# Kernel optimization log

Hardware: AMD Instinct MI355X
Metric: run time of the kernel (lower is better)

## Reference

```python
import jax, jax.numpy as jnp
import numpy as np

DN = ('NCHW', 'OIHW', 'NCHW')
BLOB_HW = 16  # hard-coded in make_gaussian_blob_maps

_ENC = [(32, 3), (32, 32), (64, 32), (64, 64), (128, 64), (128, 128), (128, 128)]
_DEC = [(64, 128), (64, 64), (32, 64), (32, 32), (16, 32), (16, 16)]


def _conv(x, w, b, stride):
    y = jax.lax.conv_general_dilated(x, w, (stride, stride), 'SAME', dimension_numbers=DN)
    return y + b[None, :, None, None]


def _tconv(x, w, b):
    # decoder stride-2 stage: 'iteratively doubling the input width'
    y = jax.lax.conv_transpose(x, w, (2, 2), 'SAME', dimension_numbers=DN)
    return y + b[None, :, None, None]


def setup_inputs() -> dict:
    key = jax.random.key(0)
    keys = jax.random.split(key, 1 + 2 * (len(_ENC) + len(_DEC)))
    inp = {'x': jax.random.normal(keys[0], (4, 8, 3, 128, 128), jnp.float32)}
    i = 1
    for j, (o, c) in enumerate(_ENC):
        inp[f'enc_w{j}'] = 0.05 * jax.random.normal(keys[i], (o, c, 3, 3), jnp.float32); i += 1
        inp[f'enc_b{j}'] = 0.05 * jax.random.normal(keys[i], (o,), jnp.float32); i += 1
    for j, (o, c) in enumerate(_DEC):
        inp[f'dec_w{j}'] = 0.05 * jax.random.normal(keys[i], (o, c, 3, 3), jnp.float32); i += 1
        inp[f'dec_b{j}'] = 0.05 * jax.random.normal(keys[i], (o,), jnp.float32); i += 1
    return inp


def _forward(x, enc_w0, enc_b0, enc_w1, enc_b1, enc_w2, enc_b2, enc_w3, enc_b3,
             enc_w4, enc_b4, enc_w5, enc_b5, enc_w6, enc_b6,
             dec_w0, dec_b0, dec_w1, dec_b1, dec_w2, dec_b2,
             dec_w3, dec_b3, dec_w4, dec_b4, dec_w5, dec_b5):
    N, T = x.shape[0], x.shape[1]
    xi = x.reshape((N * T,) + x.shape[2:])  # (B, 3, 128, 128)
    # ---- encoder ----
    h = _conv(xi, enc_w0, enc_b0, 1)                              # Identity act
    h = _conv(h, enc_w1, enc_b1, 1)                               # Identity act
    h = jax.nn.leaky_relu(_conv(h, enc_w2, enc_b2, 2), 0.2)       # 128 -> 64
    h = jax.nn.leaky_relu(_conv(h, enc_w3, enc_b3, 1), 0.2)
    h = jax.nn.leaky_relu(_conv(h, enc_w4, enc_b4, 2), 0.2)       # 64 -> 32
    h = jax.nn.leaky_relu(_conv(h, enc_w5, enc_b5, 1), 0.2)
    R = jax.nn.softplus(_conv(h, enc_w6, enc_b6, 2))              # (B, K, 16, 16)
    B, K, H, W = R.shape
    # ---- keypoint presence: mean over spatial dims ----
    mu = R.sum((2, 3)) / (H * W)                                  # (B, K)
    # ---- normalize_feature_maps: faithful net effect of the in-place loop,
    # which ends up dividing each batch item by the ORIGINAL sum of its LAST map ----
    denom = R[:, K - 1].sum((1, 2))                               # (B,)
    D = R / denom[:, None, None, None]
    # ---- average_feature_maps: spatial-index weighted sum (soft-argmax) ----
    gh = jnp.arange(H, dtype=R.dtype)
    gw = jnp.arange(W, dtype=R.dtype)
    c0 = jnp.einsum('bkhw,h->bk', D, gh)                          # row coord
    c1 = jnp.einsum('bkhw,w->bk', D, gw)                          # col coord
    # ---- gaussian blob maps: mu * exp(-0.5 * ||(u,v) - c||^2), sigma = 1 ----
    u = jnp.arange(BLOB_HW, dtype=R.dtype)[:, None]               # (16, 1)
    v = jnp.arange(BLOB_HW, dtype=R.dtype)[None, :]               # (1, 16)
    d2 = (u[None, None] - c0[:, :, None, None]) ** 2 + (v[None, None] - c1[:, :, None, None]) ** 2
    maps = mu[:, :, None, None] * jnp.exp(-0.5 * d2)              # (B, K, 16, 16)
    # ---- decoder ----
    g = jax.nn.relu(_tconv(maps, dec_w0, dec_b0))                 # 16 -> 32
    g = jax.nn.relu(_conv(g, dec_w1, dec_b1, 1))
    g = jax.nn.relu(_tconv(g, dec_w2, dec_b2))                    # 32 -> 64
    g = jax.nn.relu(_conv(g, dec_w3, dec_b3, 1))
    g = jax.nn.relu(_tconv(g, dec_w4, dec_b4))                    # 64 -> 128
    g = jax.nn.relu(_conv(g, dec_w5, dec_b5, 1))
    return g  # original forward returns the un-reshaped (N*T, C, H, W) tensor


def reference(x, enc_w0, enc_b0, enc_w1, enc_b1, enc_w2, enc_b2, enc_w3, enc_b3,
              enc_w4, enc_b4, enc_w5, enc_b5, enc_w6, enc_b6,
              dec_w0, dec_b0, dec_w1, dec_b1, dec_w2, dec_b2,
              dec_w3, dec_b3, dec_w4, dec_b4, dec_w5, dec_b5):
    return _forward(x, enc_w0, enc_b0, enc_w1, enc_b1, enc_w2, enc_b2, enc_w3, enc_b3,
                    enc_w4, enc_b4, enc_w5, enc_b5, enc_w6, enc_b6,
                    dec_w0, dec_b0, dec_w1, dec_b1, dec_w2, dec_b2,
                    dec_w3, dec_b3, dec_w4, dec_b4, dec_w5, dec_b5)
```

## Files before the change

### kernel.cpp

```cpp
#include <hip/hip_runtime.h>
#include <math.h>


enum { ACT_ID = 0, ACT_LRELU = 1, ACT_SOFTPLUS = 2, ACT_RELU = 3 };

template<int ACT>
__device__ __forceinline__ float act_fn(float x) {
  if (ACT == ACT_LRELU)    return x >= 0.f ? x : 0.2f * x;
  if (ACT == ACT_SOFTPLUS) return fmaxf(x, 0.f) + log1pf(expf(-fabsf(x)));
  if (ACT == ACT_RELU)     return fmaxf(x, 0.f);
  return x;
}

template<int ACT, int NC, int CIN>
__global__ __launch_bounds__(256)
void conv32_lds(const float* __restrict__ in, const float* __restrict__ w,
                const float* __restrict__ bias, float* __restrict__ out,
                int Cout) {
  __shared__ float pl[2][32 * 36];
  const int cogs = Cout / NC;
  const int gx  = blockIdx.x;
  const int cog = gx % cogs;
  const int b   = gx / cogs;
  const int co0 = cog * NC;
  const int t   = threadIdx.x;
  const int x0  = (t & 15) * 2;
  const int y0  = (t >> 4) * 2;

  const float* ib = in + (size_t)b * CIN * 1024;
  const int lx = (t >> 3) * 36 + (t & 7) * 4;

  {
    float4 g0 = *(const float4*)(ib + t * 4);
    *(float4*)&pl[0][lx] = g0;
  }
  __syncthreads();

  const bool okT = (y0 > 0), okB = (y0 + 2 < 32);
  const bool okL = (x0 > 0), okR = (x0 + 2 < 32);

  float acc[NC][2][2];
  #pragma unroll
  for (int u = 0; u < NC; ++u)
    #pragma unroll
    for (int o = 0; o < 2; ++o) { acc[u][o][0] = 0.f; acc[u][o][1] = 0.f; }

  int cur = 0;
  #pragma unroll 1
  for (int ci = 0; ci < CIN; ++ci) {
    const bool more = (ci + 1 < CIN);
    float4 g = {0.f, 0.f, 0.f, 0.f};
    if (more) g = *(const float4*)(ib + (size_t)(ci + 1) * 1024 + t * 4);

    const float* P = pl[cur];
    const float* wci = w + ((size_t)co0 * CIN + ci) * 9;
    #pragma unroll
    for (int r = 0; r < 4; ++r) {
      const bool ok = (r == 0) ? okT : ((r == 3) ? okB : true);
      const int ry = ok ? (y0 - 1 + r) : 0;
      const int base = ry * 36 + x0;
      float v[4];
      v[0] = (ok && okL) ? P[base - 1] : 0.f;
      v[1] = ok ? P[base]     : 0.f;
      v[2] = ok ? P[base + 1] : 0.f;
      v[3] = (ok && okR) ? P[base + 2] : 0.f;
      #pragma unroll
      for (int u = 0; u < NC; ++u) {
        const float* wp = wci + (size_t)u * CIN * 9;
        if (r <= 2) {
          const float w0 = wp[r * 3], w1 = wp[r * 3 + 1], w2 = wp[r * 3 + 2];
          acc[u][0][0] += v[0] * w0 + v[1] * w1 + v[2] * w2;
          acc[u][0][1] += v[1] * w0 + v[2] * w1 + v[3] * w2;
        }
        if (r >= 1) {
          const float w0 = wp[(r-1) * 3], w1 = wp[(r-1) * 3 + 1], w2 = wp[(r-1) * 3 + 2];
          acc[u][1][0] += v[0] * w0 + v[1] * w1 + v[2] * w2;
          acc[u][1][1] += v[1] * w0 + v[2] * w1 + v[3] * w2;
        }
      }
    }
    if (more) *(float4*)&pl[cur ^ 1][lx] = g;
    __syncthreads();
    cur ^= 1;
  }

  #pragma unroll
  for (int u = 0; u < NC; ++u) {
    const float bv = bias[co0 + u];
    float* op = out + ((size_t)(b * Cout + co0 + u) * 32 + y0) * 32 + x0;
    float2 r0, r1;
    r0.x = act_fn<ACT>(acc[u][0][0] + bv); r0.y = act_fn<ACT>(acc[u][0][1] + bv);
    r1.x = act_fn<ACT>(acc[u][1][0] + bv); r1.y = act_fn<ACT>(acc[u][1][1] + bv);
    *(float2*)op = r0;
    *(float2*)(op + 32) = r1;
  }
}

template<int ACT, int NC, int CPT, int CIN>
__global__ __launch_bounds__(256)
void conv_s1r2(const float* __restrict__ in, const float* __restrict__ w,
               const float* __restrict__ bias, float* __restrict__ out,
               int Cout, int H, int W) {
  const int cogs = Cout / NC;
  const int gx  = blockIdx.x;
  const int cog = gx % cogs;
  const int b   = gx / cogs;
  const int co0 = cog * NC;
  const int Wq  = W / CPT;
  const int Hp  = H >> 1;
  const int items = Hp * Wq;
  const int item  = blockIdx.y * 256 + threadIdx.x;
  if (item >= items) return;
  const int yp = item / Wq;
  const int x0 = (item - yp * Wq) * CPT;
  const int y0 = 2 * yp;

  const int HW = H * W;
  const float* ib = in + (size_t)b * CIN * HW;

  const bool okT = (y0 > 0), okB = (y0 + 2 < H);
  const bool okL = (x0 > 0), okR = (x0 + CPT < W);
  const int xl = okL ? (x0 - 1) : 0;
  const int xr = okR ? (x0 + CPT) : 0;

  float acc[NC][2][CPT];
  #pragma unroll
  for (int u = 0; u < NC; ++u)
    #pragma unroll
    for (int o = 0; o < 2; ++o)
      #pragma unroll
      for (int q = 0; q < CPT; ++q) acc[u][o][q] = 0.f;

  #pragma unroll 1
  for (int ci = 0; ci < CIN; ++ci) {
    const float* p = ib + ci * HW;
    const float* wci = w + ((size_t)co0 * CIN + ci) * 9;
    #pragma unroll
    for (int r = 0; r < 4; ++r) {
      const bool ok = (r == 0) ? okT : ((r == 3) ? okB : true);
      const int iy = ok ? (y0 - 1 + r) : 0;
      const float* row = p + iy * W;
      float v[CPT + 2];
      if (CPT == 4) {
        float  lf = row[xl];
        float4 m  = *(const float4*)(row + x0);
        float  rf = row[xr];
        v[0] = (ok && okL) ? lf : 0.f;
        v[1] = ok ? m.x : 0.f;
        v[2] = ok ? m.y : 0.f;
        v[3] = ok ? m.z : 0.f;
        v[4] = ok ? m.w : 0.f;
        v[5] = (ok && okR) ? rf : 0.f;
      } else if (CPT == 2) {
        float  lf = row[xl];
        float2 m  = *(const float2*)(row + x0);
        float  rf = row[xr];
        v[0] = (ok && okL) ? lf : 0.f;
        v[1] = ok ? m.x : 0.f;
        v[2] = ok ? m.y : 0.f;
        v[3] = (ok && okR) ? rf : 0.f;
      } else {
        v[0] = (ok && okL) ? row[xl] : 0.f;
        #pragma unroll
        for (int q = 0; q < CPT; ++q) v[1 + q] = ok ? row[x0 + q] : 0.f;
        v[CPT + 1] = (ok && okR) ? row[xr] : 0.f;
      }
      #pragma unroll
      for (int u = 0; u < NC; ++u) {
        const float* wp = wci + (size_t)u * CIN * 9;
        if (r <= 2) {
          const float w0 = wp[r * 3], w1 = wp[r * 3 + 1], w2 = wp[r * 3 + 2];
          #pragma unroll
          for (int q = 0; q < CPT; ++q)
            acc[u][0][q] += v[q] * w0 + v[q + 1] * w1 + v[q + 2] * w2;
        }
        if (r >= 1) {
          const float w0 = wp[(r-1) * 3], w1 = wp[(r-1) * 3 + 1], w2 = wp[(r-1) * 3 + 2];
          #pragma unroll
          for (int q = 0; q < CPT; ++q)
            acc[u][1][q] += v[q] * w0 + v[q + 1] * w1 + v[q + 2] * w2;
        }
      }
    }
  }

  #pragma unroll
  for (int u = 0; u < NC; ++u) {
    const float bv = bias[co0 + u];
    float* op = out + ((size_t)(b * Cout + co0 + u) * H + y0) * W + x0;
    #pragma unroll
    for (int o = 0; o < 2; ++o) {
      float* opo = op + o * W;
      if (CPT == 4) {
        float4 r4;
        r4.x = act_fn<ACT>(acc[u][o][0] + bv);
        r4.y = act_fn<ACT>(acc[u][o][1] + bv);
        r4.z = act_fn<ACT>(acc[u][o][2] + bv);
        r4.w = act_fn<ACT>(acc[u][o][3] + bv);
        *(float4*)opo = r4;
      } else if (CPT == 2) {
        float2 r2;
        r2.x = act_fn<ACT>(acc[u][o][0] + bv);
        r2.y = act_fn<ACT>(acc[u][o][1] + bv);
        *(float2*)opo = r2;
      } else {
        #pragma unroll
        for (int q = 0; q < CPT; ++q) opo[q] = act_fn<ACT>(acc[u][o][q] + bv);
      }
    }
  }
}

template<int ACT, int NC, int CPT, int CIN>
__global__ __launch_bounds__(256)
void conv_s1(const float* __restrict__ in, const float* __restrict__ w,
             const float* __restrict__ bias, float* __restrict__ out,
             int Cout, int H, int W) {
  const int cogs = Cout / NC;
  const int gx  = blockIdx.x;
  const int cog = gx % cogs;
  const int b   = gx / cogs;
  const int co0 = cog * NC;
  const int Wq  = W / CPT;
  const int items = H * Wq;
  const int item  = blockIdx.y * 256 + threadIdx.x;
  if (item >= items) return;
  const int y  = item / Wq;
  const int x0 = (item - y * Wq) * CPT;

  const int HW = H * W;
  const float* ib = in + (size_t)b * CIN * HW;

  const bool okT = (y > 0), okB = (y < H - 1);
  const bool okL = (x0 > 0), okR = (x0 + CPT < W);
  const int ym = okT ? (y - 1) : 0;
  const int yp = okB ? (y + 1) : 0;
  const int xl = okL ? (x0 - 1) : 0;
  const int xr = okR ? (x0 + CPT) : 0;

  float acc[NC][CPT];
  #pragma unroll
  for (int u = 0; u < NC; ++u)
    #pragma unroll
    for (int q = 0; q < CPT; ++q) acc[u][q] = 0.f;

  #pragma unroll 2
  for (int ci = 0; ci < CIN; ++ci) {
    const float* p = ib + ci * HW;
    const float* wci = w + ((size_t)co0 * CIN + ci) * 9;
    #pragma unroll
    for (int dy = 0; dy < 3; ++dy) {
      const int  ry    = (dy == 0) ? ym : ((dy == 1) ? y : yp);
      const bool okRow = (dy == 0) ? okT : ((dy == 1) ? true : okB);
      const float* r = p + ry * W;
      float v[CPT + 2];
      if (CPT == 2) {
        float  lf = r[xl];
        float2 m  = *(const float2*)(r + x0);
        float  rf = r[xr];
        v[0] = (okRow && okL) ? lf : 0.f;
        v[1] = okRow ? m.x : 0.f;
        v[2] = okRow ? m.y : 0.f;
        v[3] = (okRow && okR) ? rf : 0.f;
      } else {
        v[0] = (okRow && okL) ? r[xl] : 0.f;
        #pragma unroll
        for (int q = 0; q < CPT; ++q) v[1 + q] = okRow ? r[x0 + q] : 0.f;
        v[CPT + 1] = (okRow && okR) ? r[xr] : 0.f;
      }
      #pragma unroll
      for (int u = 0; u < NC; ++u) {
        const float* wp = wci + u * CIN * 9 + dy * 3;
        const float w0 = wp[0], w1 = wp[1], w2 = wp[2];
        #pragma unroll
        for (int q = 0; q < CPT; ++q)
          acc[u][q] += v[q] * w0 + v[q + 1] * w1 + v[q + 2] * w2;
      }
    }
  }

  #pragma unroll
  for (int u = 0; u < NC; ++u) {
    const float bv = bias[co0 + u];
    float* op = out + ((size_t)(b * Cout + co0 + u) * H + y) * W + x0;
    if (CPT == 2) {
      float2 r2;
      r2.x = act_fn<ACT>(acc[u][0] + bv);
      r2.y = act_fn<ACT>(acc[u][1] + bv);
      *(float2*)op = r2;
    } else {
      #pragma unroll
      for (int q = 0; q < CPT; ++q) op[q] = act_fn<ACT>(acc[u][q] + bv);
    }
  }
}

template<int ACT, int NC, int CPT, int CIN>
__global__ __launch_bounds__(256)
void conv_s2(const float* __restrict__ in, const float* __restrict__ w,
             const float* __restrict__ bias, float* __restrict__ out,
             int Cout, int H, int W) {
  const int Ho = H >> 1, Wo = W >> 1;
  const int cogs = Cout / NC;
  const int gx  = blockIdx.x;
  const int cog = gx % cogs;
  const int b   = gx / cogs;
  const int co0 = cog * NC;
  const int Wq  = Wo / CPT;
  const int items = Ho * Wq;
  const int item  = blockIdx.y * 256 + threadIdx.x;
  if (item >= items) return;
  const int y  = item / Wq;
  const int x0 = (item - y * Wq) * CPT;
  const int ix = 2 * x0;

  const int HW = H * W;
  const float* ib = in + (size_t)b * CIN * HW;

  const int iy0 = 2 * y, iy1 = 2 * y + 1, iy2 = 2 * y + 2;
  const bool okB = (iy2 < H);
  const int iy2c = okB ? iy2 : 0;
  const bool okR = (ix + 2 * CPT < W);
  const int ixr  = okR ? (ix + 2 * CPT) : 0;

  float acc[NC][CPT];
  #pragma unroll
  for (int u = 0; u < NC; ++u)
    #pragma unroll
    for (int q = 0; q < CPT; ++q) acc[u][q] = 0.f;

  #pragma unroll 2
  for (int ci = 0; ci < CIN; ++ci) {
    const float* p = ib + ci * HW;
    const float* wci = w + ((size_t)co0 * CIN + ci) * 9;
    #pragma unroll
    for (int dy = 0; dy < 3; ++dy) {
      const int  ry    = (dy == 0) ? iy0 : ((dy == 1) ? iy1 : iy2c);
      const bool okRow = (dy < 2) || okB;
      const float* r = p + ry * W;
      float v[2 * CPT + 1];
      if (CPT == 4) {
        float4 m0 = *(const float4*)(r + ix);
        float4 m1 = *(const float4*)(r + ix + 4);
        float  rf = r[ixr];
        v[0] = okRow ? m0.x : 0.f; v[1] = okRow ? m0.y : 0.f;
        v[2] = okRow ? m0.z : 0.f; v[3] = okRow ? m0.w : 0.f;
        v[4] = okRow ? m1.x : 0.f; v[5] = okRow ? m1.y : 0.f;
        v[6] = okRow ? m1.z : 0.f; v[7] = okRow ? m1.w : 0.f;
        v[8] = (okRow && okR) ? rf : 0.f;
      } else if (CPT == 2) {
        float4 m0 = *(const float4*)(r + ix);
        float  rf = r[ixr];
        v[0] = okRow ? m0.x : 0.f; v[1] = okRow ? m0.y : 0.f;
        v[2] = okRow ? m0.z : 0.f; v[3] = okRow ? m0.w : 0.f;
        v[4] = (okRow && okR) ? rf : 0.f;
      } else {
        float2 m0 = *(const float2*)(r + ix);
        float  rf = r[ixr];
        v[0] = okRow ? m0.x : 0.f; v[1] = okRow ? m0.y : 0.f;
        v[2] = (okRow && okR) ? rf : 0.f;
      }
      #pragma unroll
      for (int u = 0; u < NC; ++u) {
        const float* wp = wci + u * CIN * 9 + dy * 3;
        const float w0 = wp[0], w1 = wp[1], w2 = wp[2];
        #pragma unroll
        for (int q = 0; q < CPT; ++q)
          acc[u][q] += v[2*q] * w0 + v[2*q + 1] * w1 + v[2*q + 2] * w2;
      }
    }
  }

  #pragma unroll
  for (int u = 0; u < NC; ++u) {
    const float bv = bias[co0 + u];
    float* op = out + ((size_t)(b * Cout + co0 + u) * Ho + y) * Wo + x0;
    if (CPT == 4) {
      float4 r4;
      r4.x = act_fn<ACT>(acc[u][0] + bv);
      r4.y = act_fn<ACT>(acc[u][1] + bv);
      r4.z = act_fn<ACT>(acc[u][2] + bv);
      r4.w = act_fn<ACT>(acc[u][3] + bv);
      *(float4*)op = r4;
    } else if (CPT == 2) {
      float2 r2;
      r2.x = act_fn<ACT>(acc[u][0] + bv);
      r2.y = act_fn<ACT>(acc[u][1] + bv);
      *(float2*)op = r2;
    } else {
      #pragma unroll
      for (int q = 0; q < CPT; ++q) op[q] = act_fn<ACT>(acc[u][q] + bv);
    }
  }
}

template<int ACT, int NC, int CIN>
__global__ __launch_bounds__(256)
void tconv(const float* __restrict__ in, const float* __restrict__ w,
           const float* __restrict__ bias, float* __restrict__ out,
           int Cout, int Hin) {
  const int cogs = Cout / NC;
  const int gx  = blockIdx.x;
  const int cog = gx % cogs;
  const int b   = gx / cogs;
  const int co0 = cog * NC;
  const int items = Hin * Hin;
  const int item  = blockIdx.y * 256 + threadIdx.x;
  if (item >= items) return;
  const int i = item / Hin;
  const int j = item - i * Hin;

  const float* ib = in + (size_t)b * CIN * items;
  const bool okT = (i > 0), okL = (j > 0);
  const int im = okT ? i - 1 : 0;
  const int jm = okL ? j - 1 : 0;

  float a00[NC], a01[NC], a10[NC], a11[NC];
  #pragma unroll
  for (int u = 0; u < NC; ++u) { a00[u]=0.f; a01[u]=0.f; a10[u]=0.f; a11[u]=0.f; }

  #pragma unroll 2
  for (int ci = 0; ci < CIN; ++ci) {
    const float* p = ib + ci * items;
    float xtl = p[im*Hin + jm]; xtl = (okT && okL) ? xtl : 0.f;
    float xtr = p[im*Hin + j];  xtr = okT ? xtr : 0.f;
    float xbl = p[i*Hin + jm];  xbl = okL ? xbl : 0.f;
    float xbr = p[i*Hin + j];
    const float* wci = w + ((size_t)co0 * CIN + ci) * 9;
    #pragma unroll
    for (int u = 0; u < NC; ++u) {
      const float* wp = wci + u * CIN * 9;
      const float w00 = wp[0], w01 = wp[1], w02 = wp[2];
      const float w10 = wp[3], w11 = wp[4], w12 = wp[5];
      const float w20 = wp[6], w21 = wp[7], w22 = wp[8];
      a00[u] += xtl*w00 + xtr*w02 + xbl*w20 + xbr*w22;
      a01[u] += xtr*w01 + xbr*w21;
      a10[u] += xbl*w10 + xbr*w12;
      a11[u] += xbr*w11;
    }
  }

  const int Ho = Hin * 2;
  #pragma unroll
  for (int u = 0; u < NC; ++u) {
    const float bv = bias[co0 + u];
    float* op = out + (size_t)(b * Cout + co0 + u) * Ho * Ho + (2*i) * Ho + 2*j;
    float2 t0, t1;
    t0.x = act_fn<ACT>(a00[u] + bv); t0.y = act_fn<ACT>(a01[u] + bv);
    t1.x = act_fn<ACT>(a10[u] + bv); t1.y = act_fn<ACT>(a11[u] + bv);
    *(float2*)op = t0;
    *(float2*)(op + Ho) = t1;
  }
}

__global__ __launch_bounds__(64)
void kp_reduce(const float* __restrict__ R, float* __restrict__ S,
               float* __restrict__ Sh, float* __restrict__ Sw) {
  const int bk = blockIdx.x;
  const int t = threadIdx.x;
  const float* p = R + (size_t)bk * 256;
  float s = 0.f, sh = 0.f, sw = 0.f;
  #pragma unroll
  for (int q = 0; q < 4; ++q) {
    int idx = t + q * 64;
    float v = p[idx];
    s  += v;
    sh += v * (float)(idx >> 4);
    sw += v * (float)(idx & 15);
  }
  #pragma unroll
  for (int off = 32; off > 0; off >>= 1) {
    s  += __shfl_down(s, off);
    sh += __shfl_down(sh, off);
    sw += __shfl_down(sw, off);
  }
  if (t == 0) { S[bk] = s; Sh[bk] = sh; Sw[bk] = sw; }
}

__global__ __launch_bounds__(256)
void kp_maps(const float* __restrict__ S, const float* __restrict__ Sh,
             const float* __restrict__ Sw, float* __restrict__ maps, int K) {
  const int bk = blockIdx.x;
  const int b = bk / K;
  const int t = threadIdx.x;
  const float s   = S[bk];
  const float den = S[b * K + (K - 1)];
  const float mu  = s * (1.0f / 256.0f);
  const float c0  = Sh[bk] / den;
  const float c1  = Sw[bk] / den;
  const float u = (float)(t >> 4);
  const float v = (float)(t & 15);
  const float d2 = (u - c0) * (u - c0) + (v - c1) * (v - c1);
  maps[(size_t)bk * 256 + t] = mu * expf(-0.5f * d2);
}

extern "C" void kernel_launch(void* const* d_in, const int* in_sizes, int n_in,
                              void* d_out, int out_size, void* d_ws, size_t ws_size,
                              hipStream_t stream) {
  const int B = 32;
  const float* x = (const float*)d_in[0];
  const float* ew[7]; const float* eb[7];
  for (int j = 0; j < 7; ++j) { ew[j] = (const float*)d_in[1 + 2*j]; eb[j] = (const float*)d_in[2 + 2*j]; }
  const float* dw[6]; const float* db[6];
  for (int j = 0; j < 6; ++j) { dw[j] = (const float*)d_in[15 + 2*j]; db[j] = (const float*)d_in[16 + 2*j]; }

  float* ws   = (float*)d_ws;
  float* bufA = ws;
  float* bufB = bufA + 16777216;
  float* R    = bufB + 16777216;
  float* maps = R + 1048576;
  float* S    = maps + 1048576;
  float* Sh   = S + 4096;
  float* Sw   = Sh + 4096;
  float* outp = (float*)d_out;

  dim3 blk(256);

  conv_s1r2<ACT_ID,    8,4,3>  <<<dim3(B*4,   8), blk, 0, stream>>>(x,    ew[0], eb[0], bufA, 32,  128, 128);
  conv_s1r2<ACT_ID,    8,4,32> <<<dim3(B*4,   8), blk, 0, stream>>>(bufA, ew[1], eb[1], bufB, 32,  128, 128);
  conv_s2<ACT_LRELU,   8,4,32> <<<dim3(B*8,   4), blk, 0, stream>>>(bufB, ew[2], eb[2], bufA, 64,  128, 128);
  conv_s1r2<ACT_LRELU, 4,4,64> <<<dim3(B*16,  2), blk, 0, stream>>>(bufA, ew[3], eb[3], bufB, 64,  64,  64);
  conv_s2<ACT_LRELU,   8,2,64> <<<dim3(B*16,  2), blk, 0, stream>>>(bufB, ew[4], eb[4], bufA, 128, 64,  64);
  conv32_lds<ACT_LRELU,4,128>  <<<dim3(B*32),     blk, 0, stream>>>(bufA, ew[5], eb[5], bufB, 128);
  conv_s2<ACT_SOFTPLUS,4,1,128><<<dim3(B*32,  1), blk, 0, stream>>>(bufB, ew[6], eb[6], R,    128, 32,  32);

  kp_reduce<<<dim3(B*128), dim3(64), 0, stream>>>(R, S, Sh, Sw);
  kp_maps  <<<dim3(B*128), blk, 0, stream>>>(S, Sh, Sw, maps, 128);

  tconv<ACT_RELU,   2,128> <<<dim3(B*32,  1), blk, 0, stream>>>(maps, dw[0], db[0], bufA, 64, 16);
  conv_s1<ACT_RELU, 4,2,64><<<dim3(B*16,  2), blk, 0, stream>>>(bufA, dw[1], db[1], bufB, 64, 32, 32);
  tconv<ACT_RELU,   4,64>  <<<dim3(B*8,   4), blk, 0, stream>>>(bufB, dw[2], db[2], bufA, 32, 32);
  conv_s1r2<ACT_RELU,4,2,32><<<dim3(B*8,  4), blk, 0, stream>>>(bufA, dw[3], db[3], bufB, 32, 64, 64);
  tconv<ACT_RELU,   8,32>  <<<dim3(B*2,  16), blk, 0, stream>>>(bufB, dw[4], db[4], bufA, 16, 64);
  conv_s1r2<ACT_RELU,4,4,16><<<dim3(B*4,  8), blk, 0, stream>>>(bufA, dw[5], db[5], outp, 16, 128, 128);
}
```

Before: 1.192 ms.

## Add LDS-tiled double-buffered 3x3 conv kernel for large stride-1 encoder layers

Adds a generic conv_tile_lds kernel that stages a 34x34 halo tile of one input channel into double-buffered LDS while prefetching the next channel into registers. Each thread computes a 2x2 output patch for NC output channels from the shared tile. The kernel replaces conv_s1r2 for encoder layers 1 and 3. The aim is to cut redundant global loads of neighbouring pixels and overlap loads with compute, at the cost of one barrier per input channel and more LDS use.

```diff
diff --git a/kernel.cpp b/kernel.cpp
--- a/kernel.cpp
+++ b/kernel.cpp
@@ -10,6 +10,118 @@
   if (ACT == ACT_SOFTPLUS) return fmaxf(x, 0.f) + log1pf(expf(-fabsf(x)));
   if (ACT == ACT_RELU)     return fmaxf(x, 0.f);
   return x;
+}
+
+template<int ACT, int NC, int CIN, int S>
+__global__ __launch_bounds__(256)
+void conv_tile_lds(const float* __restrict__ in, const float* __restrict__ w,
+                   const float* __restrict__ bias, float* __restrict__ out,
+                   int Cout) {
+  __shared__ float pl[2][34 * 36];
+  const int TW   = S / 32;
+  const int NT   = TW * TW;
+  const int cogs = Cout / NC;
+  const int gxb  = blockIdx.x;
+  const int tile = gxb % NT;
+  const int rem  = gxb / NT;
+  const int cog  = rem % cogs;
+  const int b    = rem / cogs;
+  const int co0  = cog * NC;
+  const int tx = tile % TW, ty = tile / TW;
+  const int x00 = tx * 32, y00 = ty * 32;
+  const int t = threadIdx.x;
+
+  const float* ib = in + (size_t)b * CIN * (S * S);
+
+  int goff[5]; bool gok[5]; int lofs[5];
+  const bool t132 = (t < 132);
+  #pragma unroll
+  for (int k = 0; k < 5; ++k) {
+    const int idx = k * 256 + t;
+    const int r = idx / 34;
+    const int c = idx - r * 34;
+    lofs[k] = r * 36 + c;
+    const int gy = y00 - 1 + r;
+    const int gz = x00 - 1 + c;
+    const bool inb = (gy >= 0) && (gy < S) && (gz >= 0) && (gz < S) &&
+                     (k < 4 || t132);
+    gok[k] = inb;
+    goff[k] = inb ? (gy * S + gz) : 0;
+  }
+
+  float g[5];
+  {
+    const float* p = ib;
+    #pragma unroll
+    for (int k = 0; k < 5; ++k) { float x_ = p[goff[k]]; g[k] = gok[k] ? x_ : 0.f; }
+    #pragma unroll
+    for (int k = 0; k < 4; ++k) pl[0][lofs[k]] = g[k];
+    if (t132) pl[0][lofs[4]] = g[4];
+  }
+  __syncthreads();
+
+  const int lrow = (t >> 4) * 2;
+  const int lcol = (t & 15) * 2;
+  const int oy = y00 + (t >> 4) * 2;
+  const int ox = x00 + (t & 15) * 2;
+
+  float acc[NC][2][2];
+  #pragma unroll
+  for (int u = 0; u < NC; ++u)
+    #pragma unroll
+    for (int o = 0; o < 2; ++o) { acc[u][o][0] = 0.f; acc[u][o][1] = 0.f; }
+
+  int cur = 0;
+  #pragma unroll 1
+  for (int ci = 0; ci < CIN; ++ci) {
+    const bool more = (ci + 1 < CIN);
+    if (more) {
+      const float* p = ib + (size_t)(ci + 1) * (S * S);
+      #pragma unroll
+      for (int k = 0; k < 5; ++k) { float x_ = p[goff[k]]; g[k] = gok[k] ? x_ : 0.f; }
+    }
+
+    const float* P = pl[cur];
+    const float* wci = w + ((size_t)co0 * CIN + ci) * 9;
+    #pragma unroll
+    for (int r = 0; r < 4; ++r) {
+      const float* row = P + (lrow + r) * 36 + lcol;
+      const float v0 = row[0], v1 = row[1], v2 = row[2], v3 = row[3];
+      #pragma unroll
+      for (int u = 0; u < NC; ++u) {
+        const float* wp = wci + (size_t)u * CIN * 9;
+        if (r <= 2) {
+          const float w0 = wp[r * 3], w1 = wp[r * 3 + 1], w2 = wp[r * 3 + 2];
+          acc[u][0][0] += v0 * w0 + v1 * w1 + v2 * w2;
+          acc[u][0][1] += v1 * w0 + v2 * w1 + v3 * w2;
+        }
+        if (r >= 1) {
+          const float w0 = wp[(r-1) * 3], w1 = wp[(r-1) * 3 + 1], w2 = wp[(r-1) * 3 + 2];
+          acc[u][1][0] += v0 * w0 + v1 * w1 + v2 * w2;
+          acc[u][1][1] += v1 * w0 + v2 * w1 + v3 * w2;
+        }
+      }
+    }
+    if (more) {
+      float* dst = pl[cur ^ 1];
+      #pragma unroll
+      for (int k = 0; k < 4; ++k) dst[lofs[k]] = g[k];
+      if (t132) dst[lofs[4]] = g[4];
+    }
+    __syncthreads();
+    cur ^= 1;
+  }
+
+  #pragma unroll
+  for (int u = 0; u < NC; ++u) {
+    const float bv = bias[co0 + u];
+    float* op = out + ((size_t)(b * Cout + co0 + u) * S + oy) * S + ox;
+    float2 r0, r1;
+    r0.x = act_fn<ACT>(acc[u][0][0] + bv); r0.y = act_fn<ACT>(acc[u][0][1] + bv);
+    r1.x = act_fn<ACT>(acc[u][1][0] + bv); r1.y = act_fn<ACT>(acc[u][1][1] + bv);
+    *(float2*)op = r0;
+    *(float2*)(op + S) = r1;
+  }
 }
 
 template<int ACT, int NC, int CIN>
@@ -517,9 +629,9 @@
   dim3 blk(256);
 
   conv_s1r2<ACT_ID,    8,4,3>  <<<dim3(B*4,   8), blk, 0, stream>>>(x,    ew[0], eb[0], bufA, 32,  128, 128);
-  conv_s1r2<ACT_ID,    8,4,32> <<<dim3(B*4,   8), blk, 0, stream>>>(bufA, ew[1], eb[1], bufB, 32,  128, 128);
+  conv_tile_lds<ACT_ID,8,32,128><<<dim3(B*4*16),  blk, 0, stream>>>(bufA, ew[1], eb[1], bufB, 32);
   conv_s2<ACT_LRELU,   8,4,32> <<<dim3(B*8,   4), blk, 0, stream>>>(bufB, ew[2], eb[2], bufA, 64,  128, 128);
-  conv_s1r2<ACT_LRELU, 4,4,64> <<<dim3(B*16,  2), blk, 0, stream>>>(bufA, ew[3], eb[3], bufB, 64,  64,  64);
+  conv_tile_lds<ACT_LRELU,8,64,64><<<dim3(B*8*4), blk, 0, stream>>>(bufA, ew[3], eb[3], bufB, 64);
   conv_s2<ACT_LRELU,   8,2,64> <<<dim3(B*16,  2), blk, 0, stream>>>(bufB, ew[4], eb[4], bufA, 128, 64,  64);
   conv32_lds<ACT_LRELU,4,128>  <<<dim3(B*32),     blk, 0, stream>>>(bufA, ew[5], eb[5], bufB, 128);
   conv_s2<ACT_SOFTPLUS,4,1,128><<<dim3(B*32,  1), blk, 0, stream>>>(bufB, ew[6], eb[6], R,    128, 32,  32);
```

Result: slower. 1.225 ms (+2.7%).
